# Performance work log

Measured on AMD Instinct MI355X. Metric: run time of the kernel, lower is better.

Reference implementation:

```python
import jax, jax.numpy as jnp
import numpy as np

ALPHA = 0.6
LOSS_WEIGHT = 1.0
BIG = 1e9


def _centered_meshgrid(M):
    # centered per-cell coordinates within an MxM block, (row, col) order
    c = jnp.arange(M, dtype=jnp.float32) - (M - 1) / 2.0
    yy, xx = jnp.meshgrid(c, c, indexing='ij')
    return jnp.stack([yy, xx], axis=-1)  # [M, M, 2]


def setup_inputs() -> dict:
    key = jax.random.key(0)
    k1, k2, k3 = jax.random.split(key, 3)
    B, H, W, M, K = 4, 64, 64, 8, 64
    pred_scores = jax.random.normal(k1, (B, H * W, K), dtype=jnp.float32)
    pred_offsets = jax.random.normal(k2, (B, H * W, K, 2), dtype=jnp.float32) * 0.5
    target = jax.random.randint(k3, (B, H * M, W * M), 0, 2, dtype=jnp.int32)
    return {"pred_scores": pred_scores, "pred_offsets": pred_offsets,
            "target": target, "H": H, "W": W, "M": M}


def _forward(pred_scores, pred_offsets, target, H, W, M):
    B = target.shape[0]
    K = pred_scores.shape[-1]
    T = M * M
    HW = H * W

    tgt = (target > 0).astype(jnp.int32)
    # [B,H,M,W,M] -> [B,H,W,M,M] -> [B,HW,T]
    tgt = tgt.reshape(B, H, M, W, M).transpose(0, 1, 3, 2, 4).reshape(B, HW, T)

    # stable descending sort of targets (positives first)
    order = jnp.argsort(-tgt, axis=-1, stable=True)          # [B,HW,T]
    block_target = jnp.take_along_axis(tgt, order, axis=-1)  # [B,HW,T]

    base_off = _centered_meshgrid(M).reshape(T, 2) / M       # [T,2]
    mask_offsets = base_off[order]                           # [B,HW,T,2]

    # broadcast cost: [B,HW,K,T]
    loc_cost = jnp.abs(pred_offsets[:, :, :, None, :] - mask_offsets[:, :, None, :, :]).sum(-1)
    cls_cost = jnp.abs(jax.nn.sigmoid(pred_scores)[..., None]
                       - block_target[:, :, None, :].astype(pred_scores.dtype))
    cost = (loc_cost ** 0.8) * (cls_cost ** 0.2) * block_target[:, :, None, :].astype(pred_scores.dtype)
    cost = jax.lax.stop_gradient(cost)  # assignment is non-differentiable

    # batched greedy assignment: for each target (in sorted order) pick the
    # cheapest not-yet-assigned prediction slot
    cost_t = jnp.moveaxis(cost, -1, 0)               # [T,B,HW,K]
    assigned0 = jnp.zeros((B, HW, K), dtype=bool)
    kidx = jnp.arange(K)

    def step(assigned, c):
        c = jnp.where(assigned, BIG, c)
        idx = jnp.argmin(c, axis=-1)                 # [B,HW]
        assigned = assigned | (kidx[None, None, :] == idx[..., None])
        return assigned, idx

    _, assign = jax.lax.scan(step, assigned0, cost_t)
    assignment = jnp.moveaxis(assign, 0, -1)          # [B,HW,T] in [0,K)

    bi = jnp.arange(B)[:, None, None]
    ni = jnp.arange(HW)[None, :, None]
    target_scores = jnp.zeros((B, HW, K), jnp.int32).at[bi, ni, assignment].set(block_target)
    target_offsets = jnp.zeros_like(pred_offsets).at[bi, ni, assignment].set(
        mask_offsets.astype(pred_offsets.dtype))

    num_pos = jnp.maximum(jnp.count_nonzero(target_scores), 1).astype(pred_scores.dtype)
    # first-call EMA: old = initial = num_pos -> normalizer = num_pos
    normalizer = num_pos

    t = target_scores.astype(pred_scores.dtype)
    p = jax.nn.sigmoid(pred_scores)
    ce = -(t * jax.nn.log_sigmoid(pred_scores) + (1.0 - t) * jax.nn.log_sigmoid(-pred_scores))
    p_t = p * t + (1.0 - p) * (1.0 - t)
    focal = ce * (1.0 - p_t) ** 2 * (ALPHA * t + (1.0 - ALPHA) * (1.0 - t))
    obj_loss = focal.sum()

    loc_loss = (jnp.abs(pred_offsets - target_offsets).sum(-1) * t).sum()

    return LOSS_WEIGHT * (obj_loss / normalizer + 10.0 * loc_loss / normalizer)


def reference(pred_scores, pred_offsets, target, H, W, M):
    return _forward(pred_scores, pred_offsets, target, H, W, M)
```

## Files before the change

### kernel.cpp

```cpp
#include <hip/hip_runtime.h>
#include <math.h>

#define HW  4096
#define KK  64
#define WPB 4
#define BLK (WPB*64)

__device__ __forceinline__ float softplusf(float x) {
    return fmaxf(x, 0.0f) + log1pf(expf(-fabsf(x)));
}

__device__ __forceinline__ unsigned wave_min_u32(unsigned x) {
    asm("s_nop 1\n\t"
        "v_min_u32_dpp %0, %0, %0 row_shr:1  row_mask:0xf bank_mask:0xf\n\t"
        "s_nop 1\n\t"
        "v_min_u32_dpp %0, %0, %0 row_shr:2  row_mask:0xf bank_mask:0xf\n\t"
        "s_nop 1\n\t"
        "v_min_u32_dpp %0, %0, %0 row_shr:4  row_mask:0xf bank_mask:0xf\n\t"
        "s_nop 1\n\t"
        "v_min_u32_dpp %0, %0, %0 row_shr:8  row_mask:0xf bank_mask:0xf\n\t"
        "s_nop 1\n\t"
        "v_min_u32_dpp %0, %0, %0 row_bcast:15 row_mask:0xf bank_mask:0xf\n\t"
        "s_nop 1\n\t"
        "v_min_u32_dpp %0, %0, %0 row_bcast:31 row_mask:0xf bank_mask:0xf\n\t"
        "s_nop 1"
        : "+v"(x));
    return (unsigned)__builtin_amdgcn_readlane((int)x, 63);
}

__global__ __launch_bounds__(BLK) void assign_loss_kernel(
    const float*  __restrict__ ps,
    const float2* __restrict__ po,
    const int*    __restrict__ tgt,
    float* __restrict__ pobj,
    float* __restrict__ ploc,
    int*   __restrict__ pnp)
{
    const int lane = threadIdx.x & 63;
    const int wib  = threadIdx.x >> 6;
    const int wid  = blockIdx.x * WPB + wib;

    const int b = wid >> 12;
    const int n = wid & (HW - 1);
    const int h = n >> 6, w = n & 63;

    const int base = wid * KK + lane;
    const float  s  = ps[base];
    const float2 pv = po[base];
    const float po0 = pv.x, po1 = pv.y;

    const int ti = lane >> 3, tj = lane & 7;
    const int tv = tgt[((b * 512) + h * 8 + ti) * 512 + (w * 8 + tj)] > 0;
    const unsigned long long mask = __ballot(tv);
    const int npos = __popcll(mask);

    const float sig = 1.0f / (1.0f + expf(-s));
    const float cl  = sqrtf(sqrtf(1.0f - sig));

    unsigned long long m = mask;
    int t0 = (int)__ffsll(m) - 1;
    float by = (float)(t0 >> 3) * 0.125f - 0.4375f;
    float bx = (float)(t0 & 7)  * 0.125f - 0.4375f;
    float loc_c = fabsf(po0 - by) + fabsf(po1 - bx);
    unsigned key_c = (__float_as_uint(loc_c * cl) & ~63u) | (unsigned)lane;

    unsigned dead = 0u;
    float locl = 0.0f;

    while (m) {
        const unsigned long long m2 = m & (m - 1);
        const int t2 = (int)__ffsll(m2) - 1;
        const float by2 = (float)(t2 >> 3) * 0.125f - 0.4375f;
        const float bx2 = (float)(t2 & 7)  * 0.125f - 0.4375f;
        const float loc_n = fabsf(po0 - by2) + fabsf(po1 - bx2);
        const unsigned key_n =
            (__float_as_uint(loc_n * cl) & ~63u) | (unsigned)lane;

        const unsigned kc = key_c | dead;
        const unsigned mn = wave_min_u32(kc);
        const unsigned winner = mn & 63u;
        const bool win = ((unsigned)lane == winner);
        dead = win ? 0xFFFFFFFFu : dead;
        locl = win ? loc_c : locl;

        key_c = key_n; loc_c = loc_n; m = m2;
    }

    const bool assigned = (dead != 0u);
    const float ce  = assigned ? softplusf(-s) : softplusf(s);
    const float p_t = assigned ? sig : (1.0f - sig);
    const float om  = 1.0f - p_t;
    float focal = ce * om * om * (assigned ? 0.6f : 0.4f);
    if (!assigned) locl = 0.0f;

    float locs = locl;
    int   cnt  = npos;
    #pragma unroll
    for (int o = 32; o; o >>= 1) {
        focal += __shfl_xor(focal, o, 64);
        locs  += __shfl_xor(locs,  o, 64);
    }

    __shared__ float sobj[WPB], sloc[WPB];
    __shared__ int   snp[WPB];
    if (lane == 0) { sobj[wib] = focal; sloc[wib] = locs; snp[wib] = cnt; }
    __syncthreads();
    if (threadIdx.x == 0) {
        float o = 0.0f, l = 0.0f; int np = 0;
        #pragma unroll
        for (int q = 0; q < WPB; ++q) { o += sobj[q]; l += sloc[q]; np += snp[q]; }
        pobj[blockIdx.x] = o;
        ploc[blockIdx.x] = l;
        pnp [blockIdx.x] = np;
    }
}

__global__ __launch_bounds__(256) void finalize_kernel(
    const float* __restrict__ pobj,
    const float* __restrict__ ploc,
    const int*   __restrict__ pnp,
    int nb, float* __restrict__ out)
{
    __shared__ double so[256], sl[256];
    __shared__ long long sn[256];
    double o = 0.0, l = 0.0;
    long long np = 0;
    for (int i = threadIdx.x; i < nb; i += 256) {
        o  += (double)pobj[i];
        l  += (double)ploc[i];
        np += (long long)pnp[i];
    }
    so[threadIdx.x] = o; sl[threadIdx.x] = l; sn[threadIdx.x] = np;
    __syncthreads();
    for (int st = 128; st; st >>= 1) {
        if (threadIdx.x < st) {
            so[threadIdx.x] += so[threadIdx.x + st];
            sl[threadIdx.x] += sl[threadIdx.x + st];
            sn[threadIdx.x] += sn[threadIdx.x + st];
        }
        __syncthreads();
    }
    if (threadIdx.x == 0) {
        long long npos = sn[0] > 1 ? sn[0] : 1;
        out[0] = (float)((so[0] + 10.0 * sl[0]) / (double)npos);
    }
}

extern "C" void kernel_launch(void* const* d_in, const int* in_sizes, int n_in,
                              void* d_out, int out_size, void* d_ws, size_t ws_size,
                              hipStream_t stream) {
    const float*  ps  = (const float*)d_in[0];
    const float2* po  = (const float2*)d_in[1];
    const int*    tgt = (const int*)d_in[2];

    const int total_blocks = in_sizes[0] / KK;
    const int nwg = total_blocks / WPB;

    float* pobj = (float*)d_ws;
    float* ploc = pobj + nwg;
    int*   pnp  = (int*)(ploc + nwg);

    assign_loss_kernel<<<nwg, BLK, 0, stream>>>(ps, po, tgt, pobj, ploc, pnp);
    finalize_kernel<<<1, 256, 0, stream>>>(pobj, ploc, pnp, nwg, (float*)d_out);
}
```

Measured before the change: 34.43 us.

## Speculate four greedy assignment steps per iteration with collision fallback

The greedy assignment loop now computes keys for four consecutive positive targets and runs four independent wave-wide min reductions at once, so their latency can overlap. If any winners collide, steps 2-4 are recomputed sequentially with the earlier winners excluded. The hand-written DPP min with s_nop padding is replaced by an all-lanes butterfly min built from update_dpp, ds_swizzle and shfl_xor. In exchange, each iteration does more reduction work, and the sequential fallback adds extra reductions whenever collisions occur.

```diff
diff --git a/kernel.cpp b/kernel.cpp
--- a/kernel.cpp
+++ b/kernel.cpp
@@ -6,26 +6,21 @@
 #define WPB 4
 #define BLK (WPB*64)
 
+__device__ __forceinline__ unsigned umin32(unsigned a, unsigned b) { return a < b ? a : b; }
+
 __device__ __forceinline__ float softplusf(float x) {
     return fmaxf(x, 0.0f) + log1pf(expf(-fabsf(x)));
 }
 
-__device__ __forceinline__ unsigned wave_min_u32(unsigned x) {
-    asm("s_nop 1\n\t"
-        "v_min_u32_dpp %0, %0, %0 row_shr:1  row_mask:0xf bank_mask:0xf\n\t"
-        "s_nop 1\n\t"
-        "v_min_u32_dpp %0, %0, %0 row_shr:2  row_mask:0xf bank_mask:0xf\n\t"
-        "s_nop 1\n\t"
-        "v_min_u32_dpp %0, %0, %0 row_shr:4  row_mask:0xf bank_mask:0xf\n\t"
-        "s_nop 1\n\t"
-        "v_min_u32_dpp %0, %0, %0 row_shr:8  row_mask:0xf bank_mask:0xf\n\t"
-        "s_nop 1\n\t"
-        "v_min_u32_dpp %0, %0, %0 row_bcast:15 row_mask:0xf bank_mask:0xf\n\t"
-        "s_nop 1\n\t"
-        "v_min_u32_dpp %0, %0, %0 row_bcast:31 row_mask:0xf bank_mask:0xf\n\t"
-        "s_nop 1"
-        : "+v"(x));
-    return (unsigned)__builtin_amdgcn_readlane((int)x, 63);
+__device__ __forceinline__ unsigned allmin64(unsigned x) {
+    unsigned y;
+    y = (unsigned)__builtin_amdgcn_update_dpp((int)x,(int)x,0xB1, 0xF,0xF,false); x = umin32(x,y);
+    y = (unsigned)__builtin_amdgcn_update_dpp((int)x,(int)x,0x4E, 0xF,0xF,false); x = umin32(x,y);
+    y = (unsigned)__builtin_amdgcn_update_dpp((int)x,(int)x,0x124,0xF,0xF,false); x = umin32(x,y);
+    y = (unsigned)__builtin_amdgcn_update_dpp((int)x,(int)x,0x128,0xF,0xF,false); x = umin32(x,y);
+    y = (unsigned)__builtin_amdgcn_ds_swizzle((int)x, 0x401F);                    x = umin32(x,y);
+    y = (unsigned)__shfl_xor((int)x, 32, 64);                                     x = umin32(x,y);
+    return x;
 }
 
 __global__ __launch_bounds__(BLK) void assign_loss_kernel(
@@ -57,33 +52,71 @@
     const float sig = 1.0f / (1.0f + expf(-s));
     const float cl  = sqrtf(sqrtf(1.0f - sig));
 
-    unsigned long long m = mask;
-    int t0 = (int)__ffsll(m) - 1;
-    float by = (float)(t0 >> 3) * 0.125f - 0.4375f;
-    float bx = (float)(t0 & 7)  * 0.125f - 0.4375f;
-    float loc_c = fabsf(po0 - by) + fabsf(po1 - bx);
-    unsigned key_c = (__float_as_uint(loc_c * cl) & ~63u) | (unsigned)lane;
-
+    const unsigned lane_u = (unsigned)lane;
     unsigned dead = 0u;
     float locl = 0.0f;
 
+    unsigned long long m = mask;
     while (m) {
-        const unsigned long long m2 = m & (m - 1);
-        const int t2 = (int)__ffsll(m2) - 1;
-        const float by2 = (float)(t2 >> 3) * 0.125f - 0.4375f;
-        const float bx2 = (float)(t2 & 7)  * 0.125f - 0.4375f;
-        const float loc_n = fabsf(po0 - by2) + fabsf(po1 - bx2);
-        const unsigned key_n =
-            (__float_as_uint(loc_n * cl) & ~63u) | (unsigned)lane;
+        const int t0 = (int)__ffsll(m) - 1;  m &= m - 1;
+        const bool h1 = (m != 0);
+        const int t1 = (int)__ffsll(m) - 1;  m &= m - 1;
+        const bool h2 = (m != 0);
+        const int t2 = (int)__ffsll(m) - 1;  m &= m - 1;
+        const bool h3 = (m != 0);
+        const int t3 = (int)__ffsll(m) - 1;  m &= m - 1;
 
-        const unsigned kc = key_c | dead;
-        const unsigned mn = wave_min_u32(kc);
-        const unsigned winner = mn & 63u;
-        const bool win = ((unsigned)lane == winner);
-        dead = win ? 0xFFFFFFFFu : dead;
-        locl = win ? loc_c : locl;
+        float l0, l1, l2, l3;
+        auto cellkey = [&](int t, float& l) -> unsigned {
+            const float by = (float)(t >> 3) * 0.125f - 0.4375f;
+            const float bx = (float)(t & 7)  * 0.125f - 0.4375f;
+            l = fabsf(po0 - by) + fabsf(po1 - bx);
+            return (__float_as_uint(l * cl) & ~63u) | lane_u;
+        };
+        const unsigned k0 = cellkey(t0, l0);
+        const unsigned k1 = cellkey(t1, l1);
+        const unsigned k2 = cellkey(t2, l2);
+        const unsigned k3 = cellkey(t3, l3);
 
-        key_c = key_n; loc_c = loc_n; m = m2;
+        const unsigned e0 =  k0 | dead;
+        const unsigned e1 = (k1 | dead) | (h1 ? 0u : ~0u);
+        const unsigned e2 = (k2 | dead) | (h2 ? 0u : ~0u);
+        const unsigned e3 = (k3 | dead) | (h3 ? 0u : ~0u);
+
+        unsigned m0 = allmin64(e0);
+        unsigned m1 = allmin64(e1);
+        unsigned m2 = allmin64(e2);
+        unsigned m3 = allmin64(e3);
+
+        const unsigned w0 = (unsigned)__builtin_amdgcn_readfirstlane((int)m0) & 63u;
+        const unsigned w1 = (unsigned)__builtin_amdgcn_readfirstlane((int)m1) & 63u;
+        const unsigned w2 = (unsigned)__builtin_amdgcn_readfirstlane((int)m2) & 63u;
+        const unsigned w3 = (unsigned)__builtin_amdgcn_readfirstlane((int)m3) & 63u;
+        const bool col =
+            (h1 && (w1 == w0)) ||
+            (h2 && ((w2 == w0) || (h1 && w2 == w1))) ||
+            (h3 && ((w3 == w0) || (h1 && w3 == w1) || (h2 && w3 == w2)));
+
+        if (col) {
+            unsigned excl = (lane_u == w0) ? ~0u : 0u;
+            m1 = allmin64(e1 | excl);
+            const unsigned W1 = (unsigned)__builtin_amdgcn_readfirstlane((int)m1) & 63u;
+            if (h1) excl |= (lane_u == W1) ? ~0u : 0u;
+            m2 = allmin64(e2 | excl);
+            const unsigned W2 = (unsigned)__builtin_amdgcn_readfirstlane((int)m2) & 63u;
+            if (h2) excl |= (lane_u == W2) ? ~0u : 0u;
+            m3 = allmin64(e3 | excl);
+        }
+
+        const bool W0 = (k0 == m0);
+        const bool W1b = (k1 == m1);
+        const bool W2b = (k2 == m2);
+        const bool W3b = (k3 == m3);
+        locl = W0  ? l0 : locl;
+        locl = W1b ? l1 : locl;
+        locl = W2b ? l2 : locl;
+        locl = W3b ? l3 : locl;
+        dead = (W0 | W1b | W2b | W3b) ? ~0u : dead;
     }
 
     const bool assigned = (dead != 0u);
@@ -93,17 +126,16 @@
     float focal = ce * om * om * (assigned ? 0.6f : 0.4f);
     if (!assigned) locl = 0.0f;
 
-    float locs = locl;
-    int   cnt  = npos;
+    float fc = focal, lc = locl;
     #pragma unroll
     for (int o = 32; o; o >>= 1) {
-        focal += __shfl_xor(focal, o, 64);
-        locs  += __shfl_xor(locs,  o, 64);
+        fc += __shfl_xor(fc, o, 64);
+        lc += __shfl_xor(lc, o, 64);
     }
 
     __shared__ float sobj[WPB], sloc[WPB];
     __shared__ int   snp[WPB];
-    if (lane == 0) { sobj[wib] = focal; sloc[wib] = locs; snp[wib] = cnt; }
+    if (lane == 0) { sobj[wib] = fc; sloc[wib] = lc; snp[wib] = npos; }
     __syncthreads();
     if (threadIdx.x == 0) {
         float o = 0.0f, l = 0.0f; int np = 0;
```

Result: slower. 54.10 us (+57.1%).

## Process two blocks per wave with interleaved DPP reductions and fully unrolled target loop

Applied to the files above, without the earlier changes.

Each wave now handles two spatial blocks at once, running their greedy-assignment DPP min reductions interleaved so that one chain's latency is hidden behind the other and fewer s_nop stalls are needed. The data-dependent while loop over positive targets is replaced by a fully unrolled 64-step loop that masks non-positive targets with all-ones keys. This removes loop-carried bit scanning, but every wave now pays for all 64 reductions instead of only the roughly 32 positives. It also halves the grid size and raises register pressure.

```diff
diff --git a/kernel.cpp b/kernel.cpp
--- a/kernel.cpp
+++ b/kernel.cpp
@@ -3,29 +3,34 @@
 
 #define HW  4096
 #define KK  64
-#define WPB 4
-#define BLK (WPB*64)
+#define BLK 256
+#define BPW 2
 
 __device__ __forceinline__ float softplusf(float x) {
     return fmaxf(x, 0.0f) + log1pf(expf(-fabsf(x)));
 }
 
-__device__ __forceinline__ unsigned wave_min_u32(unsigned x) {
+__device__ __forceinline__ void wave_min2_u32(unsigned& a, unsigned& b) {
     asm("s_nop 1\n\t"
         "v_min_u32_dpp %0, %0, %0 row_shr:1  row_mask:0xf bank_mask:0xf\n\t"
-        "s_nop 1\n\t"
+        "v_min_u32_dpp %1, %1, %1 row_shr:1  row_mask:0xf bank_mask:0xf\n\t"
+        "s_nop 0\n\t"
         "v_min_u32_dpp %0, %0, %0 row_shr:2  row_mask:0xf bank_mask:0xf\n\t"
-        "s_nop 1\n\t"
+        "v_min_u32_dpp %1, %1, %1 row_shr:2  row_mask:0xf bank_mask:0xf\n\t"
+        "s_nop 0\n\t"
         "v_min_u32_dpp %0, %0, %0 row_shr:4  row_mask:0xf bank_mask:0xf\n\t"
-        "s_nop 1\n\t"
+        "v_min_u32_dpp %1, %1, %1 row_shr:4  row_mask:0xf bank_mask:0xf\n\t"
+        "s_nop 0\n\t"
         "v_min_u32_dpp %0, %0, %0 row_shr:8  row_mask:0xf bank_mask:0xf\n\t"
-        "s_nop 1\n\t"
+        "v_min_u32_dpp %1, %1, %1 row_shr:8  row_mask:0xf bank_mask:0xf\n\t"
+        "s_nop 0\n\t"
         "v_min_u32_dpp %0, %0, %0 row_bcast:15 row_mask:0xf bank_mask:0xf\n\t"
-        "s_nop 1\n\t"
+        "v_min_u32_dpp %1, %1, %1 row_bcast:15 row_mask:0xf bank_mask:0xf\n\t"
+        "s_nop 0\n\t"
         "v_min_u32_dpp %0, %0, %0 row_bcast:31 row_mask:0xf bank_mask:0xf\n\t"
+        "v_min_u32_dpp %1, %1, %1 row_bcast:31 row_mask:0xf bank_mask:0xf\n\t"
         "s_nop 1"
-        : "+v"(x));
-    return (unsigned)__builtin_amdgcn_readlane((int)x, 63);
+        : "+v"(a), "+v"(b));
 }
 
 __global__ __launch_bounds__(BLK) void assign_loss_kernel(
@@ -38,77 +43,91 @@
 {
     const int lane = threadIdx.x & 63;
     const int wib  = threadIdx.x >> 6;
-    const int wid  = blockIdx.x * WPB + wib;
+    const int wv   = blockIdx.x * 4 + wib;
+    const int A    = wv * BPW;
+    const int Bb   = A + 1;
 
-    const int b = wid >> 12;
-    const int n = wid & (HW - 1);
-    const int h = n >> 6, w = n & 63;
+    const int bA = A >> 12, nA = A & (HW - 1);
+    const int hA = nA >> 6, wA = nA & 63;
+    const int bB = Bb >> 12, nB = Bb & (HW - 1);
+    const int hB = nB >> 6, wB = nB & 63;
 
-    const int base = wid * KK + lane;
-    const float  s  = ps[base];
-    const float2 pv = po[base];
-    const float po0 = pv.x, po1 = pv.y;
+    const float  sA  = ps[A  * KK + lane];
+    const float  sB  = ps[Bb * KK + lane];
+    const float2 pvA = po[A  * KK + lane];
+    const float2 pvB = po[Bb * KK + lane];
 
     const int ti = lane >> 3, tj = lane & 7;
-    const int tv = tgt[((b * 512) + h * 8 + ti) * 512 + (w * 8 + tj)] > 0;
-    const unsigned long long mask = __ballot(tv);
-    const int npos = __popcll(mask);
+    const int tvA = tgt[((bA * 512) + hA * 8 + ti) * 512 + (wA * 8 + tj)] > 0;
+    const int tvB = tgt[((bB * 512) + hB * 8 + ti) * 512 + (wB * 8 + tj)] > 0;
+    const unsigned long long maskA = __ballot(tvA);
+    const unsigned long long maskB = __ballot(tvB);
 
-    const float sig = 1.0f / (1.0f + expf(-s));
-    const float cl  = sqrtf(sqrtf(1.0f - sig));
+    const float sigA = 1.0f / (1.0f + expf(-sA));
+    const float sigB = 1.0f / (1.0f + expf(-sB));
+    const float clA  = sqrtf(sqrtf(1.0f - sigA));
+    const float clB  = sqrtf(sqrtf(1.0f - sigB));
 
-    unsigned long long m = mask;
-    int t0 = (int)__ffsll(m) - 1;
-    float by = (float)(t0 >> 3) * 0.125f - 0.4375f;
-    float bx = (float)(t0 & 7)  * 0.125f - 0.4375f;
-    float loc_c = fabsf(po0 - by) + fabsf(po1 - bx);
-    unsigned key_c = (__float_as_uint(loc_c * cl) & ~63u) | (unsigned)lane;
+    const unsigned lane_u = (unsigned)lane;
+    unsigned deadA = 0u, deadB = 0u;
+    float loclA = 0.0f, loclB = 0.0f;
 
-    unsigned dead = 0u;
-    float locl = 0.0f;
+    #pragma unroll 64
+    for (int t = 0; t < 64; ++t) {
+        const unsigned gA = (maskA & (1ull << t)) ? 0u : ~0u;
+        const unsigned gB = (maskB & (1ull << t)) ? 0u : ~0u;
+        const float by = (float)(t >> 3) * 0.125f - 0.4375f;
+        const float bx = (float)(t & 7)  * 0.125f - 0.4375f;
 
-    while (m) {
-        const unsigned long long m2 = m & (m - 1);
-        const int t2 = (int)__ffsll(m2) - 1;
-        const float by2 = (float)(t2 >> 3) * 0.125f - 0.4375f;
-        const float bx2 = (float)(t2 & 7)  * 0.125f - 0.4375f;
-        const float loc_n = fabsf(po0 - by2) + fabsf(po1 - bx2);
-        const unsigned key_n =
-            (__float_as_uint(loc_n * cl) & ~63u) | (unsigned)lane;
+        const float lA = fabsf(pvA.x - by) + fabsf(pvA.y - bx);
+        const float lB = fabsf(pvB.x - by) + fabsf(pvB.y - bx);
+        const unsigned kA = (__float_as_uint(lA * clA) & ~63u) | lane_u;
+        const unsigned kB = (__float_as_uint(lB * clB) & ~63u) | lane_u;
 
-        const unsigned kc = key_c | dead;
-        const unsigned mn = wave_min_u32(kc);
-        const unsigned winner = mn & 63u;
-        const bool win = ((unsigned)lane == winner);
-        dead = win ? 0xFFFFFFFFu : dead;
-        locl = win ? loc_c : locl;
+        unsigned eA = (kA | deadA) | gA;
+        unsigned eB = (kB | deadB) | gB;
+        wave_min2_u32(eA, eB);
+        const unsigned mnA = (unsigned)__builtin_amdgcn_readlane((int)eA, 63);
+        const unsigned mnB = (unsigned)__builtin_amdgcn_readlane((int)eB, 63);
 
-        key_c = key_n; loc_c = loc_n; m = m2;
+        const bool wiA = (kA == mnA);
+        const bool wiB = (kB == mnB);
+        deadA = wiA ? ~0u : deadA;  loclA = wiA ? lA : loclA;
+        deadB = wiB ? ~0u : deadB;  loclB = wiB ? lB : loclB;
     }
 
-    const bool assigned = (dead != 0u);
-    const float ce  = assigned ? softplusf(-s) : softplusf(s);
-    const float p_t = assigned ? sig : (1.0f - sig);
-    const float om  = 1.0f - p_t;
-    float focal = ce * om * om * (assigned ? 0.6f : 0.4f);
-    if (!assigned) locl = 0.0f;
+    float focal = 0.0f, locs = 0.0f;
+    {
+        const bool aA = (deadA != 0u);
+        const float ceA = aA ? softplusf(-sA) : softplusf(sA);
+        const float ptA = aA ? sigA : (1.0f - sigA);
+        const float omA = 1.0f - ptA;
+        focal += ceA * omA * omA * (aA ? 0.6f : 0.4f);
+        locs  += aA ? loclA : 0.0f;
+        const bool aB = (deadB != 0u);
+        const float ceB = aB ? softplusf(-sB) : softplusf(sB);
+        const float ptB = aB ? sigB : (1.0f - sigB);
+        const float omB = 1.0f - ptB;
+        focal += ceB * omB * omB * (aB ? 0.6f : 0.4f);
+        locs  += aB ? loclB : 0.0f;
+    }
 
-    float locs = locl;
-    int   cnt  = npos;
+    float fc = focal, lc = locs;
     #pragma unroll
     for (int o = 32; o; o >>= 1) {
-        focal += __shfl_xor(focal, o, 64);
-        locs  += __shfl_xor(locs,  o, 64);
+        fc += __shfl_xor(fc, o, 64);
+        lc += __shfl_xor(lc, o, 64);
     }
+    const int cnt = __popcll(maskA) + __popcll(maskB);
 
-    __shared__ float sobj[WPB], sloc[WPB];
-    __shared__ int   snp[WPB];
-    if (lane == 0) { sobj[wib] = focal; sloc[wib] = locs; snp[wib] = cnt; }
+    __shared__ float sobj[4], sloc[4];
+    __shared__ int   snp[4];
+    if (lane == 0) { sobj[wib] = fc; sloc[wib] = lc; snp[wib] = cnt; }
     __syncthreads();
     if (threadIdx.x == 0) {
         float o = 0.0f, l = 0.0f; int np = 0;
         #pragma unroll
-        for (int q = 0; q < WPB; ++q) { o += sobj[q]; l += sloc[q]; np += snp[q]; }
+        for (int q = 0; q < 4; ++q) { o += sobj[q]; l += sloc[q]; np += snp[q]; }
         pobj[blockIdx.x] = o;
         ploc[blockIdx.x] = l;
         pnp [blockIdx.x] = np;
@@ -154,7 +173,7 @@
     const int*    tgt = (const int*)d_in[2];
 
     const int total_blocks = in_sizes[0] / KK;
-    const int nwg = total_blocks / WPB;
+    const int nwg = total_blocks / (BPW * 4);
 
     float* pobj = (float*)d_ws;
     float* ploc = pobj + nwg;
```

Measured after the change: 47.95 us. 1.39x slower.
